# Optimization experiments

Measured on AMD Instinct MI355X. Metric: run time of the kernel, lower is better.

Reference implementation:

```python
import jax, jax.numpy as jnp
import numpy as np

B, T, H, W = 4, 1024, 27, 48
LOOKUP = 101          # must be odd
OUT_DIM = 128
NBINS = 512           # 8 levels per RGB channel -> 8^3


def setup_inputs() -> dict:
    key = jax.random.key(0)
    k1, k2 = jax.random.split(key, 2)
    frames = jax.random.randint(k1, (B, T, H, W, 3), 0, 256, dtype=jnp.int32)
    # nn.Linear(lookup_window, output_dim): weight [out,in] in torch; store transposed [in,out]
    bound = 1.0 / np.sqrt(LOOKUP)
    fc_w = jax.random.uniform(k2, (LOOKUP, OUT_DIM), jnp.float32, -bound, bound)
    fc_b = jnp.zeros((OUT_DIM,), dtype=jnp.float32)
    return {"frames": frames, "fc_w": fc_w, "fc_b": fc_b}


def _color_histograms(frames):
    b, t, h, w, _ = frames.shape
    flat = frames.reshape(b * t, h * w, 3)
    # bit-pack RGB into 9-bit bin id: (R>>5)<<6 | (G>>5)<<3 | (B>>5)
    bins = ((flat[..., 0] >> 5) << 6) + ((flat[..., 1] >> 5) << 3) + (flat[..., 2] >> 5)
    bins = bins + (jnp.arange(b * t, dtype=jnp.int32) << 9)[:, None]  # per-frame offset
    hist = jax.ops.segment_sum(
        jnp.ones((b * t * h * w,), jnp.float32),
        bins.reshape(-1),
        num_segments=b * t * NBINS,
    ).reshape(b, t, NBINS)
    # F.normalize(p=2, dim=2): x / max(||x||, eps)
    norm = jnp.sqrt(jnp.sum(hist * hist, axis=2, keepdims=True))
    return hist / jnp.maximum(norm, 1e-12)


def reference(frames, fc_w, fc_b):
    x = _color_histograms(frames)             # [b, t, 512]
    b, t, _ = x.shape
    sims = jnp.einsum('bic,bjc->bij', x, x)   # [b, t, t]
    pad = (LOOKUP - 1) // 2
    sims_pad = jnp.pad(sims, ((0, 0), (0, 0), (pad, pad)))  # [b, t, t+L-1]
    # windowed gather: out[b,i,j] = sims_pad[b, i, i+j]
    row = jnp.arange(t)[:, None]                     # [t, 1]
    col = row + jnp.arange(LOOKUP)[None, :]          # [t, L]
    win = sims_pad[:, row, col]                      # [b, t, L]
    return jax.nn.relu(jnp.einsum('btl,lo->bto', win, fc_w) + fc_b)
```

## Files before the change

### kernel.cpp

```cpp
#include <hip/hip_runtime.h>
#include <math.h>

#define NB 4
#define NT 1024
#define NPIX 1296
#define NBINS 512
#define LOOKUP 101
#define PADW 50
#define ODIM 128
#define TT 4
#define WROWS (TT + 2 * PADW)

typedef _Float16 v2h __attribute__((ext_vector_type(2)));

__device__ inline float dot2(unsigned a, unsigned b, float acc) {
    union U { unsigned u; v2h h; } ua, ub;
    ua.u = a; ub.u = b;
#if __has_builtin(__builtin_amdgcn_fdot2)
    return __builtin_amdgcn_fdot2(ua.h, ub.h, acc, false);
#else
    return acc + (float)ua.h.x * (float)ub.h.x + (float)ua.h.y * (float)ub.h.y;
#endif
}

__global__ __launch_bounds__(256) void hist_kernel(const int* __restrict__ frames,
                                                   unsigned short* __restrict__ X) {
    const int frame = blockIdx.x;
    const int tid = threadIdx.x;
    __shared__ unsigned int hist[NBINS];
    for (int i = tid; i < NBINS; i += 256) hist[i] = 0u;
    __syncthreads();

    const int4* f4 = (const int4*)(frames + (size_t)frame * NPIX * 3);
    for (int g = tid; g < NPIX / 4; g += 256) {
        int4 a = f4[g * 3 + 0];
        int4 b = f4[g * 3 + 1];
        int4 c = f4[g * 3 + 2];
        int v[12] = {a.x, a.y, a.z, a.w, b.x, b.y, b.z, b.w, c.x, c.y, c.z, c.w};
#pragma unroll
        for (int p = 0; p < 4; ++p) {
            int bin = ((v[3 * p] >> 5) << 6) | ((v[3 * p + 1] >> 5) << 3) | (v[3 * p + 2] >> 5);
            atomicAdd(&hist[bin], 1u);
        }
    }
    __syncthreads();

    float local = 0.f;
    for (int i = tid; i < NBINS; i += 256) {
        float h = (float)hist[i];
        local += h * h;
    }
    for (int off = 32; off >= 1; off >>= 1) local += __shfl_xor(local, off, 64);
    __shared__ float wsum[4];
    if ((tid & 63) == 0) wsum[tid >> 6] = local;
    __syncthreads();
    float inv = 1.0f / fmaxf(sqrtf(wsum[0] + wsum[1] + wsum[2] + wsum[3]), 1e-12f);

    unsigned* xrow = (unsigned*)(X + (size_t)frame * NBINS);
    union U { _Float16 h[2]; unsigned u; } pk;
    pk.h[0] = (_Float16)((float)hist[2 * tid] * inv);
    pk.h[1] = (_Float16)((float)hist[2 * tid + 1] * inv);
    xrow[tid] = pk.u;
}

__global__ __launch_bounds__(256) void simsfc_kernel(const unsigned short* __restrict__ X,
                                                     const float* __restrict__ w,
                                                     const float* __restrict__ bias,
                                                     float* __restrict__ out) {
    const int bid = blockIdx.x;
    const int tile = ((bid & 7) << 7) | (bid >> 3);
    const int b = tile >> 8;
    const int t0 = (tile & 255) * TT;
    const int tid = threadIdx.x;
    const int gid = tid >> 4;
    const int kl = tid & 15;

    __shared__ __align__(16) uint4 st[TT][64];
    __shared__ float win_s[TT][LOOKUP + 3];

    const uint4* Xb4 = (const uint4*)(X + (size_t)b * NT * NBINS);

    {
        int dt = tid >> 6, col = tid & 63;
        st[dt][col] = Xb4[(size_t)(t0 + dt) * 64 + col];
    }
    for (int i = tid; i < TT * (LOOKUP + 3); i += 256) ((float*)win_s)[i] = 0.f;
    __syncthreads();

    uint4 tA[TT][4];
#pragma unroll
    for (int dt = 0; dt < TT; ++dt)
#pragma unroll
        for (int i = 0; i < 4; ++i) tA[dt][i] = st[dt][kl + 16 * i];

    for (int it = 0; it < 7; ++it) {
        const int joff = it * 16 + gid;
        if (joff >= WROWS) continue;
        const int j = t0 - PADW + joff;
        if (j < 0 || j >= NT) continue;
        uint4 A[4];
        const uint4* xj = Xb4 + (size_t)j * 64;
#pragma unroll
        for (int i = 0; i < 4; ++i) A[i] = xj[kl + 16 * i];
#pragma unroll
        for (int dt = 0; dt < TT; ++dt) {
            float s = 0.f;
#pragma unroll
            for (int i = 0; i < 4; ++i) {
                s = dot2(A[i].x, tA[dt][i].x, s);
                s = dot2(A[i].y, tA[dt][i].y, s);
                s = dot2(A[i].z, tA[dt][i].z, s);
                s = dot2(A[i].w, tA[dt][i].w, s);
            }
            s += __shfl_xor(s, 1, 64);
            s += __shfl_xor(s, 2, 64);
            s += __shfl_xor(s, 4, 64);
            s += __shfl_xor(s, 8, 64);
            const int l = joff - dt;
            if (kl == 0 && (unsigned)l <= 100u) win_s[dt][l] = s;
        }
    }
    __syncthreads();

    const int ch = tid & 127;
    const int g2 = tid >> 7;
    float acc0 = bias[ch], acc1 = acc0;
#pragma unroll 4
    for (int l = 0; l < LOOKUP; ++l) {
        float wv = w[l * ODIM + ch];
        acc0 = fmaf(win_s[g2][l], wv, acc0);
        acc1 = fmaf(win_s[g2 + 2][l], wv, acc1);
    }
    float* o0 = out + ((size_t)(b * NT + t0 + g2) * ODIM) + ch;
    o0[0] = fmaxf(acc0, 0.f);
    o0[2 * ODIM] = fmaxf(acc1, 0.f);
}

extern "C" void kernel_launch(void* const* d_in, const int* in_sizes, int n_in,
                              void* d_out, int out_size, void* d_ws, size_t ws_size,
                              hipStream_t stream) {
    const int*   frames = (const int*)d_in[0];
    const float* fc_w   = (const float*)d_in[1];
    const float* fc_b   = (const float*)d_in[2];
    float* out = (float*)d_out;

    unsigned short* X = (unsigned short*)d_ws;

    hist_kernel  <<<NB * NT, 256, 0, stream>>>(frames, X);
    simsfc_kernel<<<NB * NT / TT, 256, 0, stream>>>(X, fc_w, fc_b, out);
}
```

Before: 115.8 us.

## Assign one wavefront per frame in histogram kernel to remove block barriers

```diff
diff --git a/kernel.cpp b/kernel.cpp
--- a/kernel.cpp
+++ b/kernel.cpp
@@ -25,14 +25,18 @@
 
 __global__ __launch_bounds__(256) void hist_kernel(const int* __restrict__ frames,
                                                    unsigned short* __restrict__ X) {
-    const int frame = blockIdx.x;
-    const int tid = threadIdx.x;
-    __shared__ unsigned int hist[NBINS];
-    for (int i = tid; i < NBINS; i += 256) hist[i] = 0u;
-    __syncthreads();
+    const int wv = threadIdx.x >> 6;
+    const int lane = threadIdx.x & 63;
+    const int frame = blockIdx.x * 4 + wv;
+
+    __shared__ unsigned int hist[4][NBINS];
+    unsigned int* h = hist[wv];
+
+#pragma unroll
+    for (int k = 0; k < NBINS / 64; ++k) h[lane + 64 * k] = 0u;
 
     const int4* f4 = (const int4*)(frames + (size_t)frame * NPIX * 3);
-    for (int g = tid; g < NPIX / 4; g += 256) {
+    for (int g = lane; g < NPIX / 4; g += 64) {
         int4 a = f4[g * 3 + 0];
         int4 b = f4[g * 3 + 1];
         int4 c = f4[g * 3 + 2];
@@ -40,27 +44,27 @@
 #pragma unroll
         for (int p = 0; p < 4; ++p) {
             int bin = ((v[3 * p] >> 5) << 6) | ((v[3 * p + 1] >> 5) << 3) | (v[3 * p + 2] >> 5);
-            atomicAdd(&hist[bin], 1u);
+            atomicAdd(&h[bin], 1u);
         }
     }
-    __syncthreads();
 
+    float cnt[8];
     float local = 0.f;
-    for (int i = tid; i < NBINS; i += 256) {
-        float h = (float)hist[i];
-        local += h * h;
+#pragma unroll
+    for (int k = 0; k < 8; ++k) {
+        cnt[k] = (float)h[lane + 64 * k];
+        local += cnt[k] * cnt[k];
     }
     for (int off = 32; off >= 1; off >>= 1) local += __shfl_xor(local, off, 64);
-    __shared__ float wsum[4];
-    if ((tid & 63) == 0) wsum[tid >> 6] = local;
-    __syncthreads();
-    float inv = 1.0f / fmaxf(sqrtf(wsum[0] + wsum[1] + wsum[2] + wsum[3]), 1e-12f);
+    float inv = 1.0f / fmaxf(sqrtf(local), 1e-12f);
 
-    unsigned* xrow = (unsigned*)(X + (size_t)frame * NBINS);
-    union U { _Float16 h[2]; unsigned u; } pk;
-    pk.h[0] = (_Float16)((float)hist[2 * tid] * inv);
-    pk.h[1] = (_Float16)((float)hist[2 * tid + 1] * inv);
-    xrow[tid] = pk.u;
+    unsigned short* xr = X + (size_t)frame * NBINS;
+#pragma unroll
+    for (int k = 0; k < 8; ++k) {
+        union { _Float16 h16; unsigned short u; } cv;
+        cv.h16 = (_Float16)(cnt[k] * inv);
+        xr[lane + 64 * k] = cv.u;
+    }
 }
 
 __global__ __launch_bounds__(256) void simsfc_kernel(const unsigned short* __restrict__ X,
@@ -146,6 +150,6 @@
 
     unsigned short* X = (unsigned short*)d_ws;
 
-    hist_kernel  <<<NB * NT, 256, 0, stream>>>(frames, X);
+    hist_kernel  <<<NB * NT / 4, 256, 0, stream>>>(frames, X);
     simsfc_kernel<<<NB * NT / TT, 256, 0, stream>>>(X, fc_w, fc_b, out);
 }
```

Result: no change. 113.8 us (-1.7%).
